# Kernel tuning notes

Hardware: AMD Instinct MI355X
Metric: run time of the kernel (lower is better)

## Reference

```python
import jax, jax.numpy as jnp
import numpy as np

D_MODEL = 512
N = 2048
BS = 8


def setup_inputs() -> dict:
    key = jax.random.key(0)
    ks = jax.random.split(key, 5)
    inputs1 = jax.random.normal(ks[0], (BS, N, D_MODEL), dtype=jnp.float32)
    inputs2 = jax.random.normal(ks[1], (BS, N, D_MODEL), dtype=jnp.float32)
    # torch Linear weights: init.normal_(std=0.001), bias=0
    Wq = 0.001 * jax.random.normal(ks[2], (D_MODEL, D_MODEL), dtype=jnp.float32)
    Wk = 0.001 * jax.random.normal(ks[3], (D_MODEL, D_MODEL), dtype=jnp.float32)
    Wv = 0.001 * jax.random.normal(ks[4], (D_MODEL, D_MODEL), dtype=jnp.float32)
    bq = jnp.zeros((D_MODEL,), dtype=jnp.float32)
    bk = jnp.zeros((D_MODEL,), dtype=jnp.float32)
    bv = jnp.zeros((D_MODEL,), dtype=jnp.float32)
    # nn.Parameter(torch.ones((n, n)))
    position_biases = jnp.ones((N, N), dtype=jnp.float32)
    return {"inputs1": inputs1, "inputs2": inputs2, "Wq": Wq, "bq": bq,
            "Wk": Wk, "bk": bk, "Wv": Wv, "bv": bv,
            "position_biases": position_biases}


def reference(inputs1, inputs2, Wq, bq, Wk, bk, Wv, bv, position_biases):
    # torch Linear: y = x @ W.T + b
    q = inputs1 @ Wq.T + bq                     # [b, n, d]
    k = inputs1 @ Wk.T + bk                     # [b, s, d]
    v = inputs2 @ Wv.T + bv                     # [b, s, d]
    # exp(k[b,s,d] + bias[t,s]) = exp(bias)[t,s] * exp(k)[b,s,d] -> separable,
    # avoiding the original's (n, bs, n, dim) broadcast intermediate.
    expB = jnp.exp(position_biases)             # [t, s]
    ek = jnp.exp(k)                             # [b, s, d]
    num = jnp.einsum('ts,bsd->btd', expB, ek * v)
    den = jnp.einsum('ts,bsd->btd', expB, ek)
    return jax.nn.sigmoid(q) * (num / den)      # [b, n, d]
```

## Files before the change

### kernel.cpp

```cpp
#include <hip/hip_runtime.h>

typedef float  f32x4  __attribute__((ext_vector_type(4)));
typedef __bf16 bf16x8 __attribute__((ext_vector_type(8)));
typedef __bf16 bf16x4 __attribute__((ext_vector_type(4)));

#define D_MODEL 512
#define SEQ     2048
#define BATCH   8
#define ROWS    (BATCH * SEQ)

#define ASYNC_COPY16(dst_lds, src_glb)                                          \
  __builtin_amdgcn_global_load_lds(                                             \
      (const __attribute__((address_space(1))) void*)(src_glb),                 \
      (__attribute__((address_space(3))) void*)(dst_lds), 16, 0, 0)

__global__ void cvt_all_kernel(const float* __restrict__ x1,
                               const float* __restrict__ x2,
                               const float* __restrict__ posb,
                               const float* __restrict__ Wq,
                               const float* __restrict__ Wk,
                               const float* __restrict__ Wv,
                               __bf16* __restrict__ x1b, __bf16* __restrict__ x2b,
                               __bf16* __restrict__ expBb, __bf16* __restrict__ wb)
{
  const int blk = blockIdx.x;
  if (blk < 16384) {
    const float* in = (blk < 8192) ? x1 : x2;
    __bf16* out = (blk < 8192) ? x1b : x2b;
    const int i = (blk & 8191) * 256 + threadIdx.x;
    float4 v = ((const float4*)in)[i];
    bf16x4 o = { (__bf16)v.x, (__bf16)v.y, (__bf16)v.z, (__bf16)v.w };
    ((bf16x4*)out)[i] = o;
  } else if (blk < 20480) {
    const int i = (blk - 16384) * 256 + threadIdx.x;
    float4 v = ((const float4*)posb)[i];
    bf16x4 o = { (__bf16)__expf(v.x), (__bf16)__expf(v.y),
                 (__bf16)__expf(v.z), (__bf16)__expf(v.w) };
    ((bf16x4*)expBb)[i] = o;
  } else {
    const int i = (blk - 20480) * 256 + threadIdx.x;
    const int nW4 = D_MODEL * D_MODEL / 4;
    const float* src = (i < nW4) ? Wq : (i < 2 * nW4) ? Wk : Wv;
    const int ii = i - ((i < nW4) ? 0 : (i < 2 * nW4) ? nW4 : 2 * nW4);
    float4 v = ((const float4*)src)[ii];
    bf16x4 o = { (__bf16)v.x, (__bf16)v.y, (__bf16)v.z, (__bf16)v.w };
    ((bf16x4*)wb)[i] = o;
  }
}

__global__ __launch_bounds__(512) void q_gemm_kernel(
    const __bf16* __restrict__ x1b, const __bf16* __restrict__ wb,
    const float* __restrict__ bq, __bf16* __restrict__ sigq)
{
  extern __shared__ __align__(16) __bf16 smem[];

  const int K = D_MODEL;
  const int tid  = threadIdx.x;
  const int wave = tid >> 6;
  const int lane = tid & 63;
  const int quad = lane >> 4;
  const int l16  = lane & 15;
  const int wm   = (wave >> 1) * 64;
  const int wn   = (wave & 1) * 64;
  const int m0   = blockIdx.x * 256;
  const int n0   = blockIdx.y * 128;
  const int l8r  = lane >> 3;
  const int scol = ((lane & 7) ^ l8r) * 8;

  const __bf16* ga[4]; const __bf16* gb[2];
  #pragma unroll
  for (int i = 0; i < 4; ++i)
    ga[i] = x1b + (long long)(m0 + i * 64 + wave * 8 + l8r) * K + scol;
  #pragma unroll
  for (int i = 0; i < 2; ++i)
    gb[i] = wb + (long long)(n0 + i * 64 + wave * 8 + l8r) * K + scol;

  f32x4 acc[4][4];
  #pragma unroll
  for (int i = 0; i < 4; ++i)
    #pragma unroll
    for (int j = 0; j < 4; ++j) acc[i][j] = (f32x4){0.f, 0.f, 0.f, 0.f};

  auto stageA2 = [&](int c, int k0, int i0) {
    ASYNC_COPY16(smem + c * 16384 + (i0 * 64 + wave * 8) * 64, ga[i0] + k0);
    ASYNC_COPY16(smem + c * 16384 + ((i0 + 1) * 64 + wave * 8) * 64, ga[i0 + 1] + k0);
  };
  auto stageB1 = [&](int c, int k0, int i) {
    ASYNC_COPY16(smem + 32768 + c * 8192 + (i * 64 + wave * 8) * 64, gb[i] + k0);
  };

  stageA2(0, 0, 0); stageA2(0, 0, 2);
  stageB1(0, 0, 0); stageB1(0, 0, 1);

  const int s0 = ((quad    ) ^ (l16 & 7)) * 8;
  const int s1 = ((quad + 4) ^ (l16 & 7)) * 8;

  for (int t = 0; t < 8; ++t) {
    const int c = t & 1;
    asm volatile("s_waitcnt vmcnt(0)" ::: "memory");
    __builtin_amdgcn_s_barrier();
    __builtin_amdgcn_sched_barrier(0);

    const __bf16* Ac = smem +         c * 16384 + (wm + l16) * 64;
    const __bf16* Bc = smem + 32768 + c * 8192  + (wn + l16) * 64;
    const bool pf = (t + 1 < 8);
    const int k1 = (t + 1) * 64;

    bf16x8 bfr[4][2];
    #pragma unroll
    for (int p = 0; p < 2; ++p) {
      if (p == 0) {
        #pragma unroll
        for (int j = 0; j < 4; ++j) {
          bfr[j][0] = *(const bf16x8*)&Bc[j * 1024 + s0];
          bfr[j][1] = *(const bf16x8*)&Bc[j * 1024 + s1];
        }
      }
      bf16x8 af[2][2];
      #pragma unroll
      for (int ii = 0; ii < 2; ++ii) {
        af[ii][0] = *(const bf16x8*)&Ac[(p * 2 + ii) * 1024 + s0];
        af[ii][1] = *(const bf16x8*)&Ac[(p * 2 + ii) * 1024 + s1];
      }
      if (pf) {
        if (p == 0) { stageA2(c ^ 1, k1, 0); stageB1(c ^ 1, k1, 0); }
        else        { stageA2(c ^ 1, k1, 2); stageB1(c ^ 1, k1, 1); }
      }
      __builtin_amdgcn_s_barrier();
      asm volatile("s_waitcnt lgkmcnt(0)" ::: "memory");
      __builtin_amdgcn_sched_barrier(0);
      __builtin_amdgcn_s_setprio(1);
      #pragma unroll
      for (int kk = 0; kk < 2; ++kk)
        #pragma unroll
        for (int ii = 0; ii < 2; ++ii)
          #pragma unroll
          for (int j = 0; j < 4; ++j)
            acc[p * 2 + ii][j] = __builtin_amdgcn_mfma_f32_16x16x32_bf16(
                af[ii][kk], bfr[j][kk], acc[p * 2 + ii][j], 0, 0, 0);
      __builtin_amdgcn_s_setprio(0);
      __builtin_amdgcn_s_barrier();
    }
  }

  #pragma unroll
  for (int j = 0; j < 4; ++j) {
    const int col = n0 + wn + j * 16 + l16;
    const float bvv = bq[col];
    #pragma unroll
    for (int i = 0; i < 4; ++i) {
      #pragma unroll
      for (int r = 0; r < 4; ++r) {
        const int row = m0 + wm + i * 16 + quad * 4 + r;
        float x = acc[i][j][r] + bvv;
        sigq[(long long)row * D_MODEL + col] = (__bf16)(1.f / (1.f + __expf(-x)));
      }
    }
  }
}

__global__ __launch_bounds__(512) void kv_fused_kernel(
    const __bf16* __restrict__ x1b, const __bf16* __restrict__ x2b,
    const __bf16* __restrict__ wb,
    const float* __restrict__ bk, const float* __restrict__ bv,
    __bf16* __restrict__ ekvT)
{
  extern __shared__ __align__(16) __bf16 smem[];

  const int K = D_MODEL;
  const int tid  = threadIdx.x;
  const int wave = tid >> 6;
  const int lane = tid & 63;
  const int quad = lane >> 4;
  const int l16  = lane & 15;
  const int wm   = (wave >> 1) * 64;
  const int wn   = (wave & 1) * 64;
  const int F0   = blockIdx.y * 256;
  const int L0   = blockIdx.x * 128;
  const int l8r  = lane >> 3;
  const int scol = ((lane & 7) ^ l8r) * 8;
  const bool hi  = (scol >= 32);
  const int sc   = scol & 31;

  const __bf16* Wkb = wb + (long long)D_MODEL * D_MODEL;
  const __bf16* Wvb = wb + 2LL * D_MODEL * D_MODEL;

  const __bf16* gW[4]; const __bf16* gX[2];
  #pragma unroll
  for (int i = 0; i < 4; ++i)
    gW[i] = (hi ? Wvb : Wkb) + (long long)(F0 + i * 64 + wave * 8 + l8r) * K + sc;
  #pragma unroll
  for (int i = 0; i < 2; ++i)
    gX[i] = (hi ? x2b : x1b) + (long long)(L0 + i * 64 + wave * 8 + l8r) * K + sc;

  f32x4 acck[4][4], accv[4][4];
  #pragma unroll
  for (int i = 0; i < 4; ++i)
    #pragma unroll
    for (int j = 0; j < 4; ++j) {
      acck[i][j] = (f32x4){0.f, 0.f, 0.f, 0.f};
      accv[i][j] = (f32x4){0.f, 0.f, 0.f, 0.f};
    }

  auto stageW = [&](int c, int k0) {
    #pragma unroll
    for (int i = 0; i < 4; ++i)
      ASYNC_COPY16(smem + c * 16384 + (i * 64 + wave * 8) * 64, gW[i] + k0);
  };
  auto stageX = [&](int c, int k0) {
    #pragma unroll
    for (int i = 0; i < 2; ++i)
      ASYNC_COPY16(smem + 32768 + c * 8192 + (i * 64 + wave * 8) * 64, gX[i] + k0);
  };

  stageW(0, 0); stageX(0, 0);

  const int s0 = ((quad    ) ^ (l16 & 7)) * 8;
  const int s1 = ((quad + 4) ^ (l16 & 7)) * 8;

  for (int s = 0; s < 16; ++s) {
    const int c = s & 1;
    asm volatile("s_waitcnt vmcnt(0)" ::: "memory");
    __builtin_amdgcn_s_barrier();
    __builtin_amdgcn_sched_barrier(0);

    const __bf16* Wc = smem +         c * 16384 + (wm + l16) * 64;
    const __bf16* Xc = smem + 32768 + c * 8192  + (wn + l16) * 64;
    const bool pf = (s + 1 < 16);
    const int k1 = (s + 1) * 32;

    {
      bf16x8 af[4], bfr[4];
      #pragma unroll
      for (int i = 0; i < 4; ++i) af[i]  = *(const bf16x8*)&Wc[i * 1024 + s0];
      #pragma unroll
      for (int j = 0; j < 4; ++j) bfr[j] = *(const bf16x8*)&Xc[j * 1024 + s0];
      if (pf) stageW(c ^ 1, k1);
      __builtin_amdgcn_s_barrier();
      asm volatile("s_waitcnt lgkmcnt(0)" ::: "memory");
      __builtin_amdgcn_sched_barrier(0);
      __builtin_amdgcn_s_setprio(1);
      #pragma unroll
      for (int i = 0; i < 4; ++i)
        #pragma unroll
        for (int j = 0; j < 4; ++j)
          acck[i][j] = __builtin_amdgcn_mfma_f32_16x16x32_bf16(
              af[i], bfr[j], acck[i][j], 0, 0, 0);
      __builtin_amdgcn_s_setprio(0);
      __builtin_amdgcn_s_barrier();
    }
    {
      bf16x8 af[4], bfr[4];
      #pragma unroll
      for (int i = 0; i < 4; ++i) af[i]  = *(const bf16x8*)&Wc[i * 1024 + s1];
      #pragma unroll
      for (int j = 0; j < 4; ++j) bfr[j] = *(const bf16x8*)&Xc[j * 1024 + s1];
      if (pf) stageX(c ^ 1, k1);
      __builtin_amdgcn_s_barrier();
      asm volatile("s_waitcnt lgkmcnt(0)" ::: "memory");
      __builtin_amdgcn_sched_barrier(0);
      __builtin_amdgcn_s_setprio(1);
      #pragma unroll
      for (int i = 0; i < 4; ++i)
        #pragma unroll
        for (int j = 0; j < 4; ++j)
          accv[i][j] = __builtin_amdgcn_mfma_f32_16x16x32_bf16(
              af[i], bfr[j], accv[i][j], 0, 0, 0);
      __builtin_amdgcn_s_setprio(0);
      __builtin_amdgcn_s_barrier();
    }
  }

  const int b   = L0 >> 11;
  const int sb  = L0 & 2047;
  __bf16* outb = ekvT + (long long)b * (2 * D_MODEL) * SEQ + sb;
  #pragma unroll
  for (int i = 0; i < 4; ++i) {
    #pragma unroll
    for (int r = 0; r < 4; ++r) {
      const int d = F0 + wm + i * 16 + quad * 4 + r;
      const float bkd = bk[d];
      const float bvd = bv[d];
      const int gr = ((d >> 5) << 6) + (d & 31);
      #pragma unroll
      for (int j = 0; j < 4; ++j) {
        const int ss = wn + j * 16 + l16;
        const float kkv = acck[i][j][r] + bkd;
        const float vvv = accv[i][j][r] + bvd;
        const float ekf = __expf(kkv);
        outb[(long long)gr * SEQ + ss]        = (__bf16)(ekf * vvv);
        outb[(long long)(gr + 32) * SEQ + ss] = (__bf16)ekf;
      }
    }
  }
}

#define EBM 256
#define EBN 256
#define EBK 64
#define ENT (SEQ / EBK)

__global__ __launch_bounds__(512) void einsum_fused_kernel(
    const __bf16* __restrict__ A, const __bf16* __restrict__ BtAll,
    const __bf16* __restrict__ sigq, float* __restrict__ out)
{
  extern __shared__ __align__(16) __bf16 smem[];

  const int b = blockIdx.z;
  const __bf16* Bt = BtAll + (long long)b * (2 * D_MODEL) * SEQ;

  const int tid  = threadIdx.x;
  const int wave = tid >> 6;
  const int lane = tid & 63;
  const int quad = lane >> 4;
  const int l16  = lane & 15;
  const int wm   = (wave >> 2) * 128;
  const int wn   = (wave & 3) * 64;
  const int m0   = blockIdx.x * EBM;
  const int n0   = blockIdx.y * EBN;
  const int l8r  = lane >> 3;
  const int scol = ((lane & 7) ^ l8r) * 8;

  const __bf16* gA = A  + (long long)(m0 + wave * 8 + l8r) * SEQ + scol;
  const __bf16* gB = Bt + (long long)(n0 + wave * 8 + l8r) * SEQ + scol;
  __bf16* lA = smem +         (wave * 8) * 64;
  __bf16* lB = smem + 32768 + (wave * 8) * 64;

  f32x4 acc[8][4];
  #pragma unroll
  for (int i = 0; i < 8; ++i)
    #pragma unroll
    for (int j = 0; j < 4; ++j) acc[i][j] = (f32x4){0.f, 0.f, 0.f, 0.f};

  auto stage_pair = [&](int c, int k0, int i) {
    ASYNC_COPY16(lA + c * 16384 + i * 4096, gA + (long long)i * 64 * SEQ + k0);
    ASYNC_COPY16(lB + c * 16384 + i * 4096, gB + (long long)i * 64 * SEQ + k0);
  };

  #pragma unroll
  for (int i = 0; i < 4; ++i) stage_pair(0, 0, i);

  const int s0 = ((quad    ) ^ (l16 & 7)) * 8;
  const int s1 = ((quad + 4) ^ (l16 & 7)) * 8;

  for (int t = 0; t < ENT; ++t) {
    const int c = t & 1;
    asm volatile("s_waitcnt vmcnt(0)" ::: "memory");
    __builtin_amdgcn_s_barrier();
    __builtin_amdgcn_sched_barrier(0);

    const __bf16* Ac = smem +         c * 16384 + (wm + l16) * 64;
    const __bf16* Bc = smem + 32768 + c * 16384 + (wn + l16) * 64;
    const bool pf = (t + 1 < ENT);
    const int k1 = (t + 1) * EBK;

    bf16x8 bfr[4][2];
    #pragma unroll
    for (int q = 0; q < 4; ++q) {
      if (q == 0) {
        #pragma unroll
        for (int j = 0; j < 4; ++j) {
          bfr[j][0] = *(const bf16x8*)&Bc[j * 1024 + s0];
          bfr[j][1] = *(const bf16x8*)&Bc[j * 1024 + s1];
        }
      }
      bf16x8 af[2][2];
      #pragma unroll
      for (int ii = 0; ii < 2; ++ii) {
        af[ii][0] = *(const bf16x8*)&Ac[(q * 2 + ii) * 1024 + s0];
        af[ii][1] = *(const bf16x8*)&Ac[(q * 2 + ii) * 1024 + s1];
      }
      if (pf) {
        if (q == 0) { stage_pair(c ^ 1, k1, 0); stage_pair(c ^ 1, k1, 1); }
        else if (q == 1) { stage_pair(c ^ 1, k1, 2); stage_pair(c ^ 1, k1, 3); }
      }
      __builtin_amdgcn_s_barrier();
      asm volatile("s_waitcnt lgkmcnt(0)" ::: "memory");
      __builtin_amdgcn_sched_barrier(0);
      __builtin_amdgcn_s_setprio(1);
      #pragma unroll
      for (int kk = 0; kk < 2; ++kk)
        #pragma unroll
        for (int ii = 0; ii < 2; ++ii)
          #pragma unroll
          for (int j = 0; j < 4; ++j)
            acc[q * 2 + ii][j] = __builtin_amdgcn_mfma_f32_16x16x32_bf16(
                af[ii][kk], bfr[j][kk], acc[q * 2 + ii][j], 0, 0, 0);
      __builtin_amdgcn_s_setprio(0);
      __builtin_amdgcn_s_barrier();
    }
  }

  const int g = (n0 + wn) >> 6;
  #pragma unroll
  for (int j = 0; j < 2; ++j) {
    const int d = g * 32 + j * 16 + l16;
    #pragma unroll
    for (int i = 0; i < 8; ++i) {
      #pragma unroll
      for (int r = 0; r < 4; ++r) {
        const int row = m0 + wm + i * 16 + quad * 4 + r;
        const long long off = ((long long)b * SEQ + row) * D_MODEL + d;
        const float num = acc[i][j][r];
        const float den = acc[i][j + 2][r];
        out[off] = (float)sigq[off] * (num / den);
      }
    }
  }
}

extern "C" void kernel_launch(void* const* d_in, const int* in_sizes, int n_in,
                              void* d_out, int out_size, void* d_ws, size_t ws_size,
                              hipStream_t stream) {
  const float* inputs1 = (const float*)d_in[0];
  const float* inputs2 = (const float*)d_in[1];
  const float* Wq = (const float*)d_in[2];
  const float* bq = (const float*)d_in[3];
  const float* Wk = (const float*)d_in[4];
  const float* bk = (const float*)d_in[5];
  const float* Wv = (const float*)d_in[6];
  const float* bv = (const float*)d_in[7];
  const float* posb = (const float*)d_in[8];
  float* out = (float*)d_out;

  char* ws = (char*)d_ws;
  const long long szX  = (long long)ROWS * D_MODEL * 2;
  const long long szW  = (long long)D_MODEL * D_MODEL * 2;
  const long long szEB = (long long)SEQ * SEQ * 2;
  const long long szT  = (long long)BATCH * 2 * D_MODEL * SEQ * 2;
  __bf16* x1b   = (__bf16*)(ws);                 ws += szX;
  __bf16* x2b   = (__bf16*)(ws);                 ws += szX;
  __bf16* wb    = (__bf16*)(ws);                 ws += 3 * szW;
  __bf16* expBb = (__bf16*)(ws);                 ws += szEB;
  __bf16* sigq  = (__bf16*)(ws);                 ws += szX;
  __bf16* ekvT  = (__bf16*)(ws);                 ws += szT;

  static bool attr_done = false;
  if (!attr_done) {
    hipFuncSetAttribute((const void*)einsum_fused_kernel,
                        hipFuncAttributeMaxDynamicSharedMemorySize, 131072);
    hipFuncSetAttribute((const void*)q_gemm_kernel,
                        hipFuncAttributeMaxDynamicSharedMemorySize, 98304);
    hipFuncSetAttribute((const void*)kv_fused_kernel,
                        hipFuncAttributeMaxDynamicSharedMemorySize, 98304);
    attr_done = true;
  }

  cvt_all_kernel<<<21248, 256, 0, stream>>>(inputs1, inputs2, posb,
                                            Wq, Wk, Wv,
                                            x1b, x2b, expBb, wb);

  {
    dim3 g(ROWS / 256, D_MODEL / 128);
    q_gemm_kernel<<<g, 512, 98304, stream>>>(x1b, wb, bq, sigq);
  }

  {
    dim3 g(ROWS / 128, D_MODEL / 256);
    kv_fused_kernel<<<g, 512, 98304, stream>>>(x1b, x2b, wb, bk, bv, ekvT);
  }

  {
    dim3 g(SEQ / EBM, (2 * D_MODEL) / EBN, BATCH);
    einsum_fused_kernel<<<g, 512, 131072, stream>>>(expBb, ekvT, sigq, out);
  }
}
```

Baseline: 243.8 us.

## Use 4-stage BK=32 async pipeline with one barrier per k-step in einsum GEMM

Rewrites the main loop of the einsum GEMM. The k-tile shrinks from 64 to 32, the LDS double buffer becomes a 4-slot ring with three tiles in flight, and the swizzle pattern changes. Each iteration now uses counted vmcnt waits and a single barrier, replacing the per-quarter barriers and the full vmcnt(0) drain. This is meant to hide global-load latency and cut synchronisation overhead, at the cost of more loop iterations and fewer MFMAs per barrier.

```diff
diff --git a/kernel.cpp b/kernel.cpp
--- a/kernel.cpp
+++ b/kernel.cpp
@@ -295,10 +295,7 @@
   }
 }
 
-#define EBM 256
-#define EBN 256
-#define EBK 64
-#define ENT (SEQ / EBK)
+#define ENT32 (SEQ / 32)
 
 __global__ __launch_bounds__(512) void einsum_fused_kernel(
     const __bf16* __restrict__ A, const __bf16* __restrict__ BtAll,
@@ -316,15 +313,18 @@
   const int l16  = lane & 15;
   const int wm   = (wave >> 2) * 128;
   const int wn   = (wave & 3) * 64;
-  const int m0   = blockIdx.x * EBM;
-  const int n0   = blockIdx.y * EBN;
-  const int l8r  = lane >> 3;
-  const int scol = ((lane & 7) ^ l8r) * 8;
-
-  const __bf16* gA = A  + (long long)(m0 + wave * 8 + l8r) * SEQ + scol;
-  const __bf16* gB = Bt + (long long)(n0 + wave * 8 + l8r) * SEQ + scol;
-  __bf16* lA = smem +         (wave * 8) * 64;
-  __bf16* lB = smem + 32768 + (wave * 8) * 64;
+  const int m0   = blockIdx.x * 256;
+  const int n0   = blockIdx.y * 256;
+
+  const int qr = (tid >> 2) ^ ((tid >> 4) & 1);
+  const int cs = (((tid & 3) ^ (qr & 3))) * 8;
+  const __bf16* gA0 = A  + (long long)(m0 +       qr) * SEQ + cs;
+  const __bf16* gA1 = A  + (long long)(m0 + 128 + qr) * SEQ + cs;
+  const __bf16* gB0 = Bt + (long long)(n0 +       qr) * SEQ + cs;
+  const __bf16* gB1 = Bt + (long long)(n0 + 128 + qr) * SEQ + cs;
+
+  const int lxb = l16 ^ ((l16 >> 2) & 1);
+  const int sl  = (quad ^ (l16 & 3)) * 8;
 
   f32x4 acc[8][4];
   #pragma unroll
@@ -332,63 +332,45 @@
     #pragma unroll
     for (int j = 0; j < 4; ++j) acc[i][j] = (f32x4){0.f, 0.f, 0.f, 0.f};
 
-  auto stage_pair = [&](int c, int k0, int i) {
-    ASYNC_COPY16(lA + c * 16384 + i * 4096, gA + (long long)i * 64 * SEQ + k0);
-    ASYNC_COPY16(lB + c * 16384 + i * 4096, gB + (long long)i * 64 * SEQ + k0);
+  auto stage = [&](int t) {
+    const int c  = t & 3;
+    const int k0 = t * 32;
+    ASYNC_COPY16(smem +         c * 8192 +        tid * 8, gA0 + k0);
+    ASYNC_COPY16(smem +         c * 8192 + 4096 + tid * 8, gA1 + k0);
+    ASYNC_COPY16(smem + 32768 + c * 8192 +        tid * 8, gB0 + k0);
+    ASYNC_COPY16(smem + 32768 + c * 8192 + 4096 + tid * 8, gB1 + k0);
   };
 
-  #pragma unroll
-  for (int i = 0; i < 4; ++i) stage_pair(0, 0, i);
-
-  const int s0 = ((quad    ) ^ (l16 & 7)) * 8;
-  const int s1 = ((quad + 4) ^ (l16 & 7)) * 8;
-
-  for (int t = 0; t < ENT; ++t) {
-    const int c = t & 1;
-    asm volatile("s_waitcnt vmcnt(0)" ::: "memory");
+  stage(0); stage(1); stage(2);
+
+  for (int t = 0; t < ENT32; ++t) {
+    const int c = t & 3;
+    if (t < ENT32 - 2)
+      asm volatile("s_waitcnt vmcnt(8) lgkmcnt(0)" ::: "memory");
+    else if (t == ENT32 - 2)
+      asm volatile("s_waitcnt vmcnt(4) lgkmcnt(0)" ::: "memory");
+    else
+      asm volatile("s_waitcnt vmcnt(0) lgkmcnt(0)" ::: "memory");
     __builtin_amdgcn_s_barrier();
     __builtin_amdgcn_sched_barrier(0);
 
-    const __bf16* Ac = smem +         c * 16384 + (wm + l16) * 64;
-    const __bf16* Bc = smem + 32768 + c * 16384 + (wn + l16) * 64;
-    const bool pf = (t + 1 < ENT);
-    const int k1 = (t + 1) * EBK;
-
-    bf16x8 bfr[4][2];
-    #pragma unroll
-    for (int q = 0; q < 4; ++q) {
-      if (q == 0) {
-        #pragma unroll
-        for (int j = 0; j < 4; ++j) {
-          bfr[j][0] = *(const bf16x8*)&Bc[j * 1024 + s0];
-          bfr[j][1] = *(const bf16x8*)&Bc[j * 1024 + s1];
-        }
-      }
-      bf16x8 af[2][2];
-      #pragma unroll
-      for (int ii = 0; ii < 2; ++ii) {
-        af[ii][0] = *(const bf16x8*)&Ac[(q * 2 + ii) * 1024 + s0];
-        af[ii][1] = *(const bf16x8*)&Ac[(q * 2 + ii) * 1024 + s1];
-      }
-      if (pf) {
-        if (q == 0) { stage_pair(c ^ 1, k1, 0); stage_pair(c ^ 1, k1, 1); }
-        else if (q == 1) { stage_pair(c ^ 1, k1, 2); stage_pair(c ^ 1, k1, 3); }
-      }
-      __builtin_amdgcn_s_barrier();
-      asm volatile("s_waitcnt lgkmcnt(0)" ::: "memory");
-      __builtin_amdgcn_sched_barrier(0);
-      __builtin_amdgcn_s_setprio(1);
-      #pragma unroll
-      for (int kk = 0; kk < 2; ++kk)
-        #pragma unroll
-        for (int ii = 0; ii < 2; ++ii)
-          #pragma unroll
-          for (int j = 0; j < 4; ++j)
-            acc[q * 2 + ii][j] = __builtin_amdgcn_mfma_f32_16x16x32_bf16(
-                af[ii][kk], bfr[j][kk], acc[q * 2 + ii][j], 0, 0, 0);
-      __builtin_amdgcn_s_setprio(0);
-      __builtin_amdgcn_s_barrier();
-    }
+    const __bf16* Ac = smem +         c * 8192 + (wm + lxb) * 32 + sl;
+    const __bf16* Bc = smem + 32768 + c * 8192 + (wn + lxb) * 32 + sl;
+
+    bf16x8 af[8], bfr[4];
+    #pragma unroll
+    for (int i = 0; i < 8; ++i) af[i]  = *(const bf16x8*)&Ac[i * 512];
+    #pragma unroll
+    for (int j = 0; j < 4; ++j) bfr[j] = *(const bf16x8*)&Bc[j * 512];
+
+    if (t + 3 < ENT32) stage(t + 3);
+
+    #pragma unroll
+    for (int i = 0; i < 8; ++i)
+      #pragma unroll
+      for (int j = 0; j < 4; ++j)
+        acc[i][j] = __builtin_amdgcn_mfma_f32_16x16x32_bf16(
+            af[i], bfr[j], acc[i][j], 0, 0, 0);
   }
 
   const int g = (n0 + wn) >> 6;
@@ -461,7 +443,7 @@
   }
 
   {
-    dim3 g(SEQ / EBM, (2 * D_MODEL) / EBN, BATCH);
+    dim3 g(SEQ / 256, (2 * D_MODEL) / 256, BATCH);
     einsum_fused_kernel<<<g, 512, 131072, stream>>>(expBb, ekvT, sigq, out);
   }
 }
```

Result: no change. 242.8 us (-0.4%).

## Split fused K/V projection into sequential K and V passes with 64-wide K tiles

Applied to the files above, without the earlier changes.

Before, each LDS stage held 32 columns of Wk/x1 and 32 columns of Wv/x2 side by side, and both accumulators were updated every iteration. Now the K projection runs as its own pass over the full reduction, followed by a V pass, and each stage holds a 64-wide slice of a single operand pair. That halves the number of main-loop iterations and barriers per accumulator and allows B fragments to be reused across two half-steps. In exchange it adds a pipeline transition between the two passes, and the second pass re-streams the weight and input tiles from global memory.

```diff
diff --git a/kernel.cpp b/kernel.cpp
--- a/kernel.cpp
+++ b/kernel.cpp
@@ -179,19 +179,22 @@
   const int L0   = blockIdx.x * 128;
   const int l8r  = lane >> 3;
   const int scol = ((lane & 7) ^ l8r) * 8;
-  const bool hi  = (scol >= 32);
-  const int sc   = scol & 31;
 
   const __bf16* Wkb = wb + (long long)D_MODEL * D_MODEL;
   const __bf16* Wvb = wb + 2LL * D_MODEL * D_MODEL;
 
-  const __bf16* gW[4]; const __bf16* gX[2];
-  #pragma unroll
-  for (int i = 0; i < 4; ++i)
-    gW[i] = (hi ? Wvb : Wkb) + (long long)(F0 + i * 64 + wave * 8 + l8r) * K + sc;
-  #pragma unroll
-  for (int i = 0; i < 2; ++i)
-    gX[i] = (hi ? x2b : x1b) + (long long)(L0 + i * 64 + wave * 8 + l8r) * K + sc;
+  const __bf16* gWk[4]; const __bf16* gWv[4];
+  const __bf16* gX1[2]; const __bf16* gX2[2];
+  #pragma unroll
+  for (int i = 0; i < 4; ++i) {
+    gWk[i] = Wkb + (long long)(F0 + i * 64 + wave * 8 + l8r) * K + scol;
+    gWv[i] = Wvb + (long long)(F0 + i * 64 + wave * 8 + l8r) * K + scol;
+  }
+  #pragma unroll
+  for (int i = 0; i < 2; ++i) {
+    gX1[i] = x1b + (long long)(L0 + i * 64 + wave * 8 + l8r) * K + scol;
+    gX2[i] = x2b + (long long)(L0 + i * 64 + wave * 8 + l8r) * K + scol;
+  }
 
   f32x4 acck[4][4], accv[4][4];
   #pragma unroll
@@ -202,74 +205,80 @@
       accv[i][j] = (f32x4){0.f, 0.f, 0.f, 0.f};
     }
 
-  auto stageW = [&](int c, int k0) {
-    #pragma unroll
-    for (int i = 0; i < 4; ++i)
-      ASYNC_COPY16(smem + c * 16384 + (i * 64 + wave * 8) * 64, gW[i] + k0);
-  };
-  auto stageX = [&](int c, int k0) {
-    #pragma unroll
-    for (int i = 0; i < 2; ++i)
-      ASYNC_COPY16(smem + 32768 + c * 8192 + (i * 64 + wave * 8) * 64, gX[i] + k0);
-  };
-
-  stageW(0, 0); stageX(0, 0);
+  auto stgW = [&](int c, int i, const __bf16* p) {
+    ASYNC_COPY16(smem + c * 16384 + (i * 64 + wave * 8) * 64, p);
+  };
+  auto stgX = [&](int c, int i, const __bf16* p) {
+    ASYNC_COPY16(smem + 32768 + c * 8192 + (i * 64 + wave * 8) * 64, p);
+  };
+
+  stgW(0, 0, gWk[0]); stgW(0, 1, gWk[1]); stgW(0, 2, gWk[2]); stgW(0, 3, gWk[3]);
+  stgX(0, 0, gX1[0]); stgX(0, 1, gX1[1]);
 
   const int s0 = ((quad    ) ^ (l16 & 7)) * 8;
   const int s1 = ((quad + 4) ^ (l16 & 7)) * 8;
 
-  for (int s = 0; s < 16; ++s) {
-    const int c = s & 1;
-    asm volatile("s_waitcnt vmcnt(0)" ::: "memory");
-    __builtin_amdgcn_s_barrier();
-    __builtin_amdgcn_sched_barrier(0);
-
-    const __bf16* Wc = smem +         c * 16384 + (wm + l16) * 64;
-    const __bf16* Xc = smem + 32768 + c * 8192  + (wn + l16) * 64;
-    const bool pf = (s + 1 < 16);
-    const int k1 = (s + 1) * 32;
-
-    {
-      bf16x8 af[4], bfr[4];
-      #pragma unroll
-      for (int i = 0; i < 4; ++i) af[i]  = *(const bf16x8*)&Wc[i * 1024 + s0];
-      #pragma unroll
-      for (int j = 0; j < 4; ++j) bfr[j] = *(const bf16x8*)&Xc[j * 1024 + s0];
-      if (pf) stageW(c ^ 1, k1);
+  auto pass = [&](f32x4 (&acc)[4][4], bool vpass) {
+    for (int t = 0; t < 8; ++t) {
+      const int c = t & 1;
+      asm volatile("s_waitcnt vmcnt(0)" ::: "memory");
       __builtin_amdgcn_s_barrier();
-      asm volatile("s_waitcnt lgkmcnt(0)" ::: "memory");
       __builtin_amdgcn_sched_barrier(0);
-      __builtin_amdgcn_s_setprio(1);
-      #pragma unroll
-      for (int i = 0; i < 4; ++i)
-        #pragma unroll
-        for (int j = 0; j < 4; ++j)
-          acck[i][j] = __builtin_amdgcn_mfma_f32_16x16x32_bf16(
-              af[i], bfr[j], acck[i][j], 0, 0, 0);
-      __builtin_amdgcn_s_setprio(0);
-      __builtin_amdgcn_s_barrier();
-    }
-    {
-      bf16x8 af[4], bfr[4];
-      #pragma unroll
-      for (int i = 0; i < 4; ++i) af[i]  = *(const bf16x8*)&Wc[i * 1024 + s1];
-      #pragma unroll
-      for (int j = 0; j < 4; ++j) bfr[j] = *(const bf16x8*)&Xc[j * 1024 + s1];
-      if (pf) stageX(c ^ 1, k1);
-      __builtin_amdgcn_s_barrier();
-      asm volatile("s_waitcnt lgkmcnt(0)" ::: "memory");
-      __builtin_amdgcn_sched_barrier(0);
-      __builtin_amdgcn_s_setprio(1);
-      #pragma unroll
-      for (int i = 0; i < 4; ++i)
-        #pragma unroll
-        for (int j = 0; j < 4; ++j)
-          accv[i][j] = __builtin_amdgcn_mfma_f32_16x16x32_bf16(
-              af[i], bfr[j], accv[i][j], 0, 0, 0);
-      __builtin_amdgcn_s_setprio(0);
-      __builtin_amdgcn_s_barrier();
-    }
-  }
+
+      const __bf16* Ac = smem +         c * 16384 + (wm + l16) * 64;
+      const __bf16* Bc = smem + 32768 + c * 8192  + (wn + l16) * 64;
+      const bool nx = (t == 7);
+      const bool pf = !(vpass && nx);
+      const bool sv = vpass || nx;
+      const int k1 = nx ? 0 : (t + 1) * 64;
+
+      bf16x8 bfr[4][2];
+      #pragma unroll
+      for (int p = 0; p < 2; ++p) {
+        if (p == 0) {
+          #pragma unroll
+          for (int j = 0; j < 4; ++j) {
+            bfr[j][0] = *(const bf16x8*)&Bc[j * 1024 + s0];
+            bfr[j][1] = *(const bf16x8*)&Bc[j * 1024 + s1];
+          }
+        }
+        bf16x8 af[2][2];
+        #pragma unroll
+        for (int ii = 0; ii < 2; ++ii) {
+          af[ii][0] = *(const bf16x8*)&Ac[(p * 2 + ii) * 1024 + s0];
+          af[ii][1] = *(const bf16x8*)&Ac[(p * 2 + ii) * 1024 + s1];
+        }
+        if (pf) {
+          if (p == 0) {
+            stgW(c ^ 1, 0, (sv ? gWv[0] : gWk[0]) + k1);
+            stgW(c ^ 1, 1, (sv ? gWv[1] : gWk[1]) + k1);
+            stgX(c ^ 1, 0, (sv ? gX2[0] : gX1[0]) + k1);
+          } else {
+            stgW(c ^ 1, 2, (sv ? gWv[2] : gWk[2]) + k1);
+            stgW(c ^ 1, 3, (sv ? gWv[3] : gWk[3]) + k1);
+            stgX(c ^ 1, 1, (sv ? gX2[1] : gX1[1]) + k1);
+          }
+        }
+        __builtin_amdgcn_s_barrier();
+        asm volatile("s_waitcnt lgkmcnt(0)" ::: "memory");
+        __builtin_amdgcn_sched_barrier(0);
+        __builtin_amdgcn_s_setprio(1);
+        #pragma unroll
+        for (int kk = 0; kk < 2; ++kk)
+          #pragma unroll
+          for (int ii = 0; ii < 2; ++ii)
+            #pragma unroll
+            for (int j = 0; j < 4; ++j)
+              acc[p * 2 + ii][j] = __builtin_amdgcn_mfma_f32_16x16x32_bf16(
+                  af[ii][kk], bfr[j][kk], acc[p * 2 + ii][j], 0, 0, 0);
+        __builtin_amdgcn_s_setprio(0);
+        __builtin_amdgcn_s_barrier();
+      }
+    }
+  };
+
+  pass(acck, false);
+  pass(accv, true);
 
   const int b   = L0 >> 11;
   const int sb  = L0 & 2047;
```

After: 239.5 us. About the same (-1.8%).
